# Kernel optimization log

Hardware: AMD Instinct MI355X
Metric: run time of the kernel (lower is better)

## Reference

```python
import jax, jax.numpy as jnp
import numpy as np

P, H_OUT, D, NX = 32, 1, 256, 16
S_A = -0.1

def layernorm(x, g, b, eps=1e-5):
    mu = jnp.mean(x, axis=-1, keepdims=True)
    var = jnp.var(x, axis=-1, keepdims=True)
    return (x - mu) * jax.lax.rsqrt(var + eps) * g + b

def setup_inputs() -> dict:
    key = jax.random.key(0)
    ks = jax.random.split(key, 16)
    B, L = 8, 2048
    y = jax.random.normal(ks[0], (B, L, P), jnp.float32)
    Win = jax.random.normal(ks[1], (P, D), jnp.float32) / np.sqrt(P)
    bin_ = jnp.zeros((D,), jnp.float32)
    ng = jnp.ones((D,), jnp.float32); nb = jnp.zeros((D,), jnp.float32)
    # A = -10*rand + s_A, with A[:,0] = s_A (fix first state of each channel)
    A = -10.0 * jax.random.uniform(ks[2], (D, NX), jnp.float32) + S_A
    A = A.at[:, 0].set(S_A)
    W_B = jax.random.normal(ks[3], (NX, D), jnp.float32)
    W_C = jax.random.normal(ks[4], (NX, D), jnp.float32)
    q_delta = jax.random.normal(ks[5], (D,), jnp.float32)
    p_delta = jax.random.normal(ks[6], (1,), jnp.float32)
    nfg = jnp.ones((D,), jnp.float32); nfb = jnp.zeros((D,), jnp.float32)
    W1 = jax.random.normal(ks[7], (D, D), jnp.float32) / np.sqrt(D)
    b1 = jnp.zeros((D,), jnp.float32)
    W2 = jax.random.normal(ks[8], (D, H_OUT * P), jnp.float32) / np.sqrt(D)
    b2 = jnp.zeros((H_OUT * P,), jnp.float32)
    return {"y": y, "Win": Win, "bin_": bin_, "ng": ng, "nb": nb, "A": A,
            "W_B": W_B, "W_C": W_C, "q_delta": q_delta, "p_delta": p_delta,
            "nfg": nfg, "nfb": nfb, "W1": W1, "b1": b1, "W2": W2, "b2": b2}

def selective_scan(u, delta, A, Bm, Cm):
    # u: (B,L,D), delta: (B,L), A: (D,NX), Bm/Cm: (B,L,NX)
    dA = jnp.exp(delta[..., None, None] * A)                      # (B,L,D,NX)
    dBu = delta[..., None, None] * Bm[:, :, None, :] * u[..., None]  # (B,L,D,NX)
    x0 = jnp.zeros((u.shape[0], u.shape[2], A.shape[1]), u.dtype)
    def step(x, inp):
        dA_t, dBu_t, C_t = inp
        x = dA_t * x + dBu_t                                      # (B,D,NX)
        y_t = jnp.einsum('bdn,bn->bd', x, C_t)
        return x, y_t
    _, ys = jax.lax.scan(step, x0, (dA.transpose(1, 0, 2, 3),
                                    dBu.transpose(1, 0, 2, 3),
                                    Cm.transpose(1, 0, 2)))
    return ys.transpose(1, 0, 2)                                  # (B,L,D)

def reference(y, Win, bin_, ng, nb, A, W_B, W_C, q_delta, p_delta,
              nfg, nfb, W1, b1, W2, b2):
    B, L, _ = y.shape
    h = y @ Win + bin_                                            # (B,L,D)
    hn = layernorm(h, ng, nb)
    delta = jax.nn.softplus(p_delta[0] + jnp.einsum('bld,d->bl', hn, q_delta))
    Bm = jnp.einsum('nd,bld->bln', W_B, hn)
    Cm = jnp.einsum('nd,bld->bln', W_C, hn)
    upd = selective_scan(hn, delta, A, Bm, Cm)
    h = h + upd
    h = layernorm(h, nfg, nfb)
    out = jax.nn.gelu(h @ W1 + b1, approximate=False) @ W2 + b2
    return out.reshape(B, L, H_OUT, P)
```

## Files before the change

### kernel.cpp

```cpp
#include <hip/hip_runtime.h>
#include <math.h>

#define D 256
#define NX 16
#define L 2048
#define NBATCH 8
#define NTOK (NBATCH * L)
#define CL 32
#define NCH (L / CL)
#define LOG2E 1.44269504088896340736f

typedef float f32x4 __attribute__((ext_vector_type(4)));
typedef short bf16x8 __attribute__((ext_vector_type(8)));

__device__ __forceinline__ unsigned short f2bf(float x) {
  unsigned u = __float_as_uint(x);
  u = u + 0x7fffu + ((u >> 16) & 1u);
  return (unsigned short)(u >> 16);
}
__device__ __forceinline__ float bf2f(unsigned short h) {
  return __uint_as_float(((unsigned)h) << 16);
}

__global__ __launch_bounds__(256) void k0_prep(const float* __restrict__ A,
                                               const float* __restrict__ WB,
                                               const float* __restrict__ WC,
                                               const float* __restrict__ W1,
                                               const float* __restrict__ W2,
                                               float* __restrict__ At,
                                               float* __restrict__ Wbct,
                                               unsigned short* __restrict__ W1fh,
                                               unsigned short* __restrict__ W1fl,
                                               unsigned short* __restrict__ W2fh,
                                               unsigned short* __restrict__ W2fl) {
  int i = blockIdx.x * 256 + threadIdx.x;
  if (i < 4096) {
    int d = i >> 4, n = i & 15;
    At[n * D + d] = A[i] * LOG2E;
  } else if (i < 12288) {
    int j = i - 4096;
    int d = j >> 5, c = j & 31;
    Wbct[j] = (c < 16) ? WB[c * D + d] : WC[(c - 16) * D + d];
  } else if (i < 77824) {
    int e = i - 12288;
    int j = e & 7, l = (e >> 3) & 63, tt = (e >> 9) & 15, s = e >> 13;
    int k = s * 32 + ((l >> 4) << 3) + j;
    int n = tt * 16 + (l & 15);
    float x = W1[k * 256 + n];
    unsigned short h = f2bf(x);
    W1fh[e] = h;
    W1fl[e] = f2bf(x - bf2f(h));
  } else {
    int e = i - 77824;
    int j = e & 7, l = (e >> 3) & 63, tt = (e >> 9) & 1, s = e >> 10;
    int k = s * 32 + ((l >> 4) << 3) + j;
    int n = tt * 16 + (l & 15);
    float x = W2[k * 32 + n];
    unsigned short h = f2bf(x);
    W2fh[e] = h;
    W2fl[e] = f2bf(x - bf2f(h));
  }
}

__global__ __launch_bounds__(512, 4) void k1a_front_scan(
    const float* __restrict__ y, const float* __restrict__ Win,
    const float* __restrict__ bin_, const float* __restrict__ ng,
    const float* __restrict__ nb, const float* __restrict__ Wbct,
    const float* __restrict__ qd, const float* __restrict__ pd,
    const float* __restrict__ At,
    float* __restrict__ hn, float* __restrict__ delta,
    float* __restrict__ Bm, float* __restrict__ Cm,
    float* __restrict__ muv, float* __restrict__ irsv,
    float* __restrict__ EX, float* __restrict__ T) {
  __shared__ float sy[32][32];
  __shared__ float sh[32][260];
  __shared__ float sB[32][NX];
  __shared__ float sdelta[32];
  __shared__ float sph[2 * 32 * 32];
  int t = threadIdx.x;
  int tok0 = blockIdx.x * 32;
  if (t < 256) {
    const float4* src = (const float4*)(y + (size_t)tok0 * 32);
    ((float4*)sy)[t] = src[t];
  }
  __syncthreads();
  int dcol = t & 63;
  int jrow = t >> 6;
  int d4 = dcol * 4;
  float4 bv = ((const float4*)bin_)[dcol];
  float4 g4 = ((const float4*)ng)[dcol];
  float4 nb4 = ((const float4*)nb)[dcol];
  float4 q4 = ((const float4*)qd)[dcol];
  float pd0 = pd[0];
  const float4* Win4 = (const float4*)Win;
  for (int g = 0; g < 2; ++g) {
    int j0 = jrow * 4 + g * 2;
    float4 acc0 = bv, acc1 = bv;
    #pragma unroll 4
    for (int k = 0; k < 32; ++k) {
      float4 wv = Win4[k * 64 + dcol];
      float a0 = sy[j0][k];
      float a1 = sy[j0 + 1][k];
      acc0.x = fmaf(a0, wv.x, acc0.x); acc1.x = fmaf(a1, wv.x, acc1.x);
      acc0.y = fmaf(a0, wv.y, acc0.y); acc1.y = fmaf(a1, wv.y, acc1.y);
      acc0.z = fmaf(a0, wv.z, acc0.z); acc1.z = fmaf(a1, wv.z, acc1.z);
      acc0.w = fmaf(a0, wv.w, acc0.w); acc1.w = fmaf(a1, wv.w, acc1.w);
    }
    #pragma unroll
    for (int p = 0; p < 2; ++p) {
      int j = j0 + p;
      int tok = tok0 + j;
      float4 a = (p == 0) ? acc0 : acc1;
      float s1 = a.x + a.y + a.z + a.w;
      float s2 = a.x * a.x + a.y * a.y + a.z * a.z + a.w * a.w;
      #pragma unroll
      for (int off = 1; off < 64; off <<= 1) {
        s1 += __shfl_xor(s1, off);
        s2 += __shfl_xor(s2, off);
      }
      float mu = s1 * (1.f / D);
      float var = s2 * (1.f / D) - mu * mu;
      float rstd = rsqrtf(var + 1e-5f);
      if (dcol == 0) { muv[tok] = mu; irsv[tok] = sqrtf(var + 1e-5f); }
      float4 v4;
      v4.x = (a.x - mu) * rstd * g4.x + nb4.x;
      v4.y = (a.y - mu) * rstd * g4.y + nb4.y;
      v4.z = (a.z - mu) * rstd * g4.z + nb4.z;
      v4.w = (a.w - mu) * rstd * g4.w + nb4.w;
      ((float4*)(hn + (size_t)tok * D))[dcol] = v4;
      *(float4*)&sh[j][d4] = v4;
      float dd = v4.x * q4.x + v4.y * q4.y + v4.z * q4.z + v4.w * q4.w;
      #pragma unroll
      for (int off = 1; off < 64; off <<= 1) dd += __shfl_xor(dd, off);
      if (dcol == 0) {
        float xx = pd0 + dd;
        float dv = (xx > 20.f) ? xx : log1pf(expf(xx));
        delta[tok] = dv;
        sdelta[j] = dv;
      }
    }
  }
  __syncthreads();
  if (t < 32) {
    float v = sdelta[t];
    #pragma unroll
    for (int off = 1; off < 32; off <<= 1) v += __shfl_xor(v, off);
    if (t == 0) T[blockIdx.x] = v;
  }
  {
    int hk = t >> 8;
    int r = t & 255;
    int col4 = r & 7;
    int j = r >> 3;
    const float* shrow = &sh[j][hk * 128];
    const float4* W4 = (const float4*)Wbct + (size_t)hk * 128 * 8;
    float4 o = make_float4(0.f, 0.f, 0.f, 0.f);
    #pragma unroll 4
    for (int k = 0; k < 128; ++k) {
      float av = shrow[k];
      float4 wv = W4[k * 8 + col4];
      o.x = fmaf(av, wv.x, o.x);
      o.y = fmaf(av, wv.y, o.y);
      o.z = fmaf(av, wv.z, o.z);
      o.w = fmaf(av, wv.w, o.w);
    }
    *(float4*)&sph[((hk * 32 + j) << 5) + col4 * 4] = o;
  }
  __syncthreads();
  if (t < 256) {
    int j = t >> 3, cc = t & 7;
    float4 r0 = *(float4*)&sph[(j << 5) + cc * 4];
    float4 r1 = *(float4*)&sph[((32 + j) << 5) + cc * 4];
    float4 r;
    r.x = r0.x + r1.x; r.y = r0.y + r1.y;
    r.z = r0.z + r1.z; r.w = r0.w + r1.w;
    int tokj = tok0 + j;
    if (cc < 4) {
      ((float4*)(Bm + (size_t)tokj * NX))[cc] = r;
      *(float4*)&sB[j][cc * 4] = r;
    } else {
      ((float4*)(Cm + (size_t)tokj * NX))[cc - 4] = r;
    }
  }
  __syncthreads();
  {
    int half = t >> 8;
    int d = t & 255;
    float a8[8], x8[8];
    #pragma unroll
    for (int n = 0; n < 8; ++n) {
      a8[n] = At[(half * 8 + n) * D + d];
      x8[n] = 0.f;
    }
    for (int lo = 0; lo < CL; ++lo) {
      float dlt = sdelta[lo];
      float du = dlt * sh[lo][d];
      #pragma unroll
      for (int n = 0; n < 8; ++n)
        x8[n] = fmaf(exp2f(dlt * a8[n]), x8[n], du * sB[lo][half * 8 + n]);
    }
    size_t exbase = (size_t)blockIdx.x * (NX * D) + d;
    #pragma unroll
    for (int n = 0; n < 8; ++n) EX[exbase + (half * 8 + n) * D] = x8[n];
  }
}

__global__ __launch_bounds__(64) void k2b_chunkscan(
    const float* __restrict__ At, const float* __restrict__ T,
    float* __restrict__ EX) {
  __shared__ float sT[NCH];
  int b = blockIdx.x >> 6;
  int rem = ((blockIdx.x & 63) << 6) | threadIdx.x;
  sT[threadIdx.x] = T[b * NCH + threadIdx.x];
  __syncthreads();
  float A2 = At[rem];
  size_t base = ((size_t)b << 18) + rem;
  float eq[8];
  #pragma unroll
  for (int j = 0; j < 8; ++j) eq[j] = EX[base + ((size_t)j << 12)];
  float x = 0.f;
  #pragma unroll 8
  for (int c = 0; c < NCH; ++c) {
    float e = eq[c & 7];
    if (c + 8 < NCH) eq[c & 7] = EX[base + ((size_t)(c + 8) << 12)];
    EX[base + ((size_t)c << 12)] = x;
    x = fmaf(exp2f(sT[c] * A2), x, e);
  }
}

__device__ __forceinline__ float gelu_exact(float x) {
  return 0.5f * x * (1.f + erff(x * 0.70710678118654752440f));
}

__global__ __launch_bounds__(256) void k2cd_scan_mlp(
    const float* __restrict__ hn, const float* __restrict__ delta,
    const float* __restrict__ Bm, const float* __restrict__ Cm,
    const float* __restrict__ At, const float* __restrict__ EX,
    const float* __restrict__ muv, const float* __restrict__ irsv,
    const float* __restrict__ ng, const float* __restrict__ nb,
    const float* __restrict__ nfg, const float* __restrict__ nfb,
    const unsigned short* __restrict__ W1fh, const unsigned short* __restrict__ W1fl,
    const unsigned short* __restrict__ W2fh, const unsigned short* __restrict__ W2fl,
    const float* __restrict__ b1, const float* __restrict__ b2,
    float* __restrict__ out) {
  __shared__ float s_az[32 * 260];
  __shared__ __align__(16) unsigned short sAh[32 * 256];
  __shared__ __align__(16) unsigned short sAl[32 * 256];
  __shared__ float sB[32][NX];
  __shared__ float sC[32][NX];
  __shared__ float sdelta[32];
  __shared__ float smu[32];
  __shared__ float sirs[32];
  int t = threadIdx.x;
  int tok0 = blockIdx.x * 32;
  size_t tokbase = (size_t)tok0;
  if (t < 32) {
    sdelta[t] = delta[tokbase + t];
    smu[t] = muv[tokbase + t];
    sirs[t] = irsv[tokbase + t];
  }
  for (int i = t; i < 32 * NX; i += 256) {
    ((float*)sB)[i] = Bm[tokbase * NX + i];
    ((float*)sC)[i] = Cm[tokbase * NX + i];
  }
  float a16[16], x16[16];
  size_t exbase = (size_t)blockIdx.x * (NX * D) + t;
  #pragma unroll
  for (int n = 0; n < 16; ++n) {
    a16[n] = At[n * D + t];
    x16[n] = EX[exbase + n * D];
  }
  float nb_d = nb[t];
  float invg = 1.0f / ng[t];
  __syncthreads();
  for (int lo = 0; lo < CL; ++lo) {
    float hv = hn[(tokbase + lo) * D + t];
    float dlt = sdelta[lo];
    float du = dlt * hv;
    float p = 0.f;
    #pragma unroll
    for (int n = 0; n < 16; ++n) {
      x16[n] = fmaf(exp2f(dlt * a16[n]), x16[n], du * sB[lo][n]);
      p = fmaf(x16[n], sC[lo][n], p);
    }
    float h = fmaf((hv - nb_d) * invg, sirs[lo], smu[lo]);
    s_az[lo * 260 + t] = h + p;
  }
  __syncthreads();
  int dcol = t & 63, jrow = t >> 6;
  int d4 = dcol * 4, j8 = jrow * 8;
  {
    float4 g4 = ((const float4*)nfg)[dcol];
    float4 b4 = ((const float4*)nfb)[dcol];
    for (int jj = 0; jj < 8; ++jj) {
      int lo = j8 + jj;
      float4 v = *(float4*)&s_az[lo * 260 + d4];
      float s1 = v.x + v.y + v.z + v.w;
      float s2 = v.x * v.x + v.y * v.y + v.z * v.z + v.w * v.w;
      #pragma unroll
      for (int off = 1; off < 64; off <<= 1) {
        s1 += __shfl_xor(s1, off);
        s2 += __shfl_xor(s2, off);
      }
      float mu2 = s1 * (1.f / D);
      float var2 = s2 * (1.f / D) - mu2 * mu2;
      float rstd2 = rsqrtf(var2 + 1e-5f);
      float4 o;
      o.x = (v.x - mu2) * rstd2 * g4.x + b4.x;
      o.y = (v.y - mu2) * rstd2 * g4.y + b4.y;
      o.z = (v.z - mu2) * rstd2 * g4.z + b4.z;
      o.w = (v.w - mu2) * rstd2 * g4.w + b4.w;
      unsigned short h0 = f2bf(o.x), h1 = f2bf(o.y), h2 = f2bf(o.z), h3 = f2bf(o.w);
      unsigned short q0 = f2bf(o.x - bf2f(h0));
      unsigned short q1 = f2bf(o.y - bf2f(h1));
      unsigned short q2 = f2bf(o.z - bf2f(h2));
      unsigned short q3 = f2bf(o.w - bf2f(h3));
      unsigned off16 = ((unsigned)(d4 * 2)) ^ ((unsigned)(lo & 7) << 4);
      uint2 hv2, lv2;
      hv2.x = (unsigned)h0 | ((unsigned)h1 << 16);
      hv2.y = (unsigned)h2 | ((unsigned)h3 << 16);
      lv2.x = (unsigned)q0 | ((unsigned)q1 << 16);
      lv2.y = (unsigned)q2 | ((unsigned)q3 << 16);
      *(uint2*)((char*)sAh + lo * 512 + off16) = hv2;
      *(uint2*)((char*)sAl + lo * 512 + off16) = lv2;
    }
  }
  __syncthreads();
  int l = t & 63, w = t >> 6;
  const bf16x8* B1h = (const bf16x8*)W1fh;
  const bf16x8* B1l = (const bf16x8*)W1fl;
  f32x4 acc[2][4];
  #pragma unroll
  for (int m = 0; m < 2; ++m)
    #pragma unroll
    for (int n = 0; n < 4; ++n) {
      f32x4 z4 = {0.f, 0.f, 0.f, 0.f};
      acc[m][n] = z4;
    }
  #pragma unroll 2
  for (int s = 0; s < 8; ++s) {
    bf16x8 ah[2], al[2];
    #pragma unroll
    for (int m = 0; m < 2; ++m) {
      int row = m * 16 + (l & 15);
      unsigned off16 = ((unsigned)(s * 64 + ((l >> 4) << 4))) ^ ((unsigned)(row & 7) << 4);
      ah[m] = *(const bf16x8*)((const char*)sAh + row * 512 + off16);
      al[m] = *(const bf16x8*)((const char*)sAl + row * 512 + off16);
    }
    #pragma unroll
    for (int n = 0; n < 4; ++n) {
      int bi = (s * 16 + w * 4 + n) * 64 + l;
      bf16x8 bh = B1h[bi];
      bf16x8 bl = B1l[bi];
      #pragma unroll
      for (int m = 0; m < 2; ++m) {
        acc[m][n] = __builtin_amdgcn_mfma_f32_16x16x32_bf16(ah[m], bh, acc[m][n], 0, 0, 0);
        acc[m][n] = __builtin_amdgcn_mfma_f32_16x16x32_bf16(al[m], bh, acc[m][n], 0, 0, 0);
        acc[m][n] = __builtin_amdgcn_mfma_f32_16x16x32_bf16(ah[m], bl, acc[m][n], 0, 0, 0);
        acc[m][n] = __builtin_amdgcn_mfma_f32_16x16x32_bf16(al[m], bl, acc[m][n], 0, 0, 0);
      }
    }
  }
  __syncthreads();
  #pragma unroll
  for (int n = 0; n < 4; ++n) {
    int colz = w * 64 + n * 16 + (l & 15);
    float b1v = b1[colz];
    #pragma unroll
    for (int m = 0; m < 2; ++m) {
      #pragma unroll
      for (int r = 0; r < 4; ++r) {
        int row = m * 16 + ((l >> 4) << 2) + r;
        float zv = gelu_exact(acc[m][n][r] + b1v);
        unsigned short zh = f2bf(zv);
        unsigned short zl = f2bf(zv - bf2f(zh));
        unsigned off16 = ((unsigned)(colz * 2)) ^ ((unsigned)(row & 7) << 4);
        *(unsigned short*)((char*)sAh + row * 512 + off16) = zh;
        *(unsigned short*)((char*)sAl + row * 512 + off16) = zl;
      }
    }
  }
  __syncthreads();
  int mw = w >> 1, nw = w & 1;
  const bf16x8* B2h = (const bf16x8*)W2fh;
  const bf16x8* B2l = (const bf16x8*)W2fl;
  f32x4 acc2 = {0.f, 0.f, 0.f, 0.f};
  #pragma unroll 2
  for (int s = 0; s < 8; ++s) {
    int row = mw * 16 + (l & 15);
    unsigned off16 = ((unsigned)(s * 64 + ((l >> 4) << 4))) ^ ((unsigned)(row & 7) << 4);
    bf16x8 zh8 = *(const bf16x8*)((const char*)sAh + row * 512 + off16);
    bf16x8 zl8 = *(const bf16x8*)((const char*)sAl + row * 512 + off16);
    int bi = (s * 2 + nw) * 64 + l;
    bf16x8 bh = B2h[bi];
    bf16x8 bl = B2l[bi];
    acc2 = __builtin_amdgcn_mfma_f32_16x16x32_bf16(zh8, bh, acc2, 0, 0, 0);
    acc2 = __builtin_amdgcn_mfma_f32_16x16x32_bf16(zl8, bh, acc2, 0, 0, 0);
    acc2 = __builtin_amdgcn_mfma_f32_16x16x32_bf16(zh8, bl, acc2, 0, 0, 0);
    acc2 = __builtin_amdgcn_mfma_f32_16x16x32_bf16(zl8, bl, acc2, 0, 0, 0);
  }
  int colo = nw * 16 + (l & 15);
  float b2v = b2[colo];
  #pragma unroll
  for (int r = 0; r < 4; ++r) {
    int row = mw * 16 + ((l >> 4) << 2) + r;
    out[(size_t)(tok0 + row) * 32 + colo] = acc2[r] + b2v;
  }
}

extern "C" void kernel_launch(void* const* d_in, const int* in_sizes, int n_in,
                              void* d_out, int out_size, void* d_ws, size_t ws_size,
                              hipStream_t stream) {
  const float* y    = (const float*)d_in[0];
  const float* Win  = (const float*)d_in[1];
  const float* bin_ = (const float*)d_in[2];
  const float* ng   = (const float*)d_in[3];
  const float* nb   = (const float*)d_in[4];
  const float* A    = (const float*)d_in[5];
  const float* WB   = (const float*)d_in[6];
  const float* WC   = (const float*)d_in[7];
  const float* qd   = (const float*)d_in[8];
  const float* pd   = (const float*)d_in[9];
  const float* nfg  = (const float*)d_in[10];
  const float* nfb  = (const float*)d_in[11];
  const float* W1   = (const float*)d_in[12];
  const float* b1   = (const float*)d_in[13];
  const float* W2   = (const float*)d_in[14];
  const float* b2   = (const float*)d_in[15];

  float* ws = (float*)d_ws;
  float* hnbuf = ws;
  float* delta = ws + 4194304;
  float* Bm    = delta + NTOK;
  float* Cm    = Bm + NTOK * NX;
  float* muv   = Cm + NTOK * NX;
  float* irsv  = muv + NTOK;
  float* Tbuf  = irsv + NTOK;
  float* At    = Tbuf + NBATCH * NCH;
  float* Wbct  = At + D * NX;
  float* EX    = Wbct + D * 32;
  unsigned short* W1fh = (unsigned short*)(EX + 2097152);
  unsigned short* W1fl = W1fh + 65536;
  unsigned short* W2fh = W1fl + 65536;
  unsigned short* W2fl = W2fh + 8192;

  k0_prep<<<336, 256, 0, stream>>>(A, WB, WC, W1, W2, At, Wbct,
                                   W1fh, W1fl, W2fh, W2fl);
  k1a_front_scan<<<NTOK / 32, 512, 0, stream>>>(y, Win, bin_, ng, nb, Wbct,
                                                qd, pd, At, hnbuf, delta, Bm,
                                                Cm, muv, irsv, EX, Tbuf);
  k2b_chunkscan<<<NBATCH * 64, 64, 0, stream>>>(At, Tbuf, EX);
  k2cd_scan_mlp<<<NTOK / 32, 256, 0, stream>>>(hnbuf, delta, Bm, Cm, At, EX,
                                               muv, irsv, ng, nb, nfg, nfb,
                                               W1fh, W1fl, W2fh, W2fl,
                                               b1, b2, (float*)d_out);
}
```

Measured before the change: 199.4 us.

## Move front-end input projection and B/C projection onto split-bf16 MFMA

Replaces the scalar FMA input projection (y@Win) and the hn@[W_B;W_C] projection in the front-scan kernel with 16x16x32 bf16 MFMA using hi/lo bf16 splits (four MFMAs per tile) to keep near-fp32 accuracy. The prep kernel now builds pre-swizzled hi/lo bf16 fragments for Win and W_B/W_C. LayerNorm statistics and the delta dot product are reduced through shared memory across waves, and hn is staged into XOR-swizzled bf16 shared buffers for the second GEMM. The aim is to cut ALU time in the front kernel, at the cost of extra conversions, more shared memory (which may lower occupancy) and more barriers.

```diff
diff --git a/kernel.cpp b/kernel.cpp
--- a/kernel.cpp
+++ b/kernel.cpp
@@ -25,24 +25,43 @@
 __global__ __launch_bounds__(256) void k0_prep(const float* __restrict__ A,
                                                const float* __restrict__ WB,
                                                const float* __restrict__ WC,
+                                               const float* __restrict__ Win,
                                                const float* __restrict__ W1,
                                                const float* __restrict__ W2,
                                                float* __restrict__ At,
-                                               float* __restrict__ Wbct,
                                                unsigned short* __restrict__ W1fh,
                                                unsigned short* __restrict__ W1fl,
                                                unsigned short* __restrict__ W2fh,
-                                               unsigned short* __restrict__ W2fl) {
+                                               unsigned short* __restrict__ W2fl,
+                                               unsigned short* __restrict__ Winfh,
+                                               unsigned short* __restrict__ Winfl,
+                                               unsigned short* __restrict__ Wbcfh,
+                                               unsigned short* __restrict__ Wbcfl) {
   int i = blockIdx.x * 256 + threadIdx.x;
   if (i < 4096) {
     int d = i >> 4, n = i & 15;
     At[n * D + d] = A[i] * LOG2E;
   } else if (i < 12288) {
-    int j = i - 4096;
-    int d = j >> 5, c = j & 31;
-    Wbct[j] = (c < 16) ? WB[c * D + d] : WC[(c - 16) * D + d];
-  } else if (i < 77824) {
+    int e = i - 4096;
+    int j = e & 7, l = (e >> 3) & 63, tt = e >> 9;
+    int k = ((l >> 4) << 3) + j;
+    int n = tt * 16 + (l & 15);
+    float x = Win[k * 256 + n];
+    unsigned short h = f2bf(x);
+    Winfh[e] = h;
+    Winfl[e] = f2bf(x - bf2f(h));
+  } else if (i < 20480) {
     int e = i - 12288;
+    int j = e & 7, l = (e >> 3) & 63, q = e >> 9;
+    int s = q >> 1, tt = q & 1;
+    int k = s * 32 + ((l >> 4) << 3) + j;
+    int n = tt * 16 + (l & 15);
+    float x = (n < 16) ? WB[n * 256 + k] : WC[(n - 16) * 256 + k];
+    unsigned short h = f2bf(x);
+    Wbcfh[e] = h;
+    Wbcfl[e] = f2bf(x - bf2f(h));
+  } else if (i < 86016) {
+    int e = i - 20480;
     int j = e & 7, l = (e >> 3) & 63, tt = (e >> 9) & 15, s = e >> 13;
     int k = s * 32 + ((l >> 4) << 3) + j;
     int n = tt * 16 + (l & 15);
@@ -51,7 +70,7 @@
     W1fh[e] = h;
     W1fl[e] = f2bf(x - bf2f(h));
   } else {
-    int e = i - 77824;
+    int e = i - 86016;
     int j = e & 7, l = (e >> 3) & 63, tt = (e >> 9) & 1, s = e >> 10;
     int k = s * 32 + ((l >> 4) << 3) + j;
     int n = tt * 16 + (l & 15);
@@ -63,123 +82,225 @@
 }
 
 __global__ __launch_bounds__(512, 4) void k1a_front_scan(
-    const float* __restrict__ y, const float* __restrict__ Win,
-    const float* __restrict__ bin_, const float* __restrict__ ng,
-    const float* __restrict__ nb, const float* __restrict__ Wbct,
+    const float* __restrict__ y, const float* __restrict__ bin_,
+    const float* __restrict__ ng, const float* __restrict__ nb,
     const float* __restrict__ qd, const float* __restrict__ pd,
     const float* __restrict__ At,
+    const unsigned short* __restrict__ Winfh,
+    const unsigned short* __restrict__ Winfl,
+    const unsigned short* __restrict__ Wbcfh,
+    const unsigned short* __restrict__ Wbcfl,
     float* __restrict__ hn, float* __restrict__ delta,
     float* __restrict__ Bm, float* __restrict__ Cm,
     float* __restrict__ muv, float* __restrict__ irsv,
     float* __restrict__ EX, float* __restrict__ T) {
-  __shared__ float sy[32][32];
+  __shared__ float sy[32][36];
   __shared__ float sh[32][260];
   __shared__ float sB[32][NX];
+  __shared__ float sred[32][16];
   __shared__ float sdelta[32];
-  __shared__ float sph[2 * 32 * 32];
+  __shared__ float smu[32];
+  __shared__ float srstd[32];
+  __shared__ __align__(16) unsigned short sChA_h[32 * 256];
+  __shared__ __align__(16) unsigned short sChA_l[32 * 256];
   int t = threadIdx.x;
+  int l = t & 63;
+  int w = t >> 6;
   int tok0 = blockIdx.x * 32;
   if (t < 256) {
-    const float4* src = (const float4*)(y + (size_t)tok0 * 32);
-    ((float4*)sy)[t] = src[t];
-  }
-  __syncthreads();
-  int dcol = t & 63;
-  int jrow = t >> 6;
-  int d4 = dcol * 4;
-  float4 bv = ((const float4*)bin_)[dcol];
-  float4 g4 = ((const float4*)ng)[dcol];
-  float4 nb4 = ((const float4*)nb)[dcol];
-  float4 q4 = ((const float4*)qd)[dcol];
-  float pd0 = pd[0];
-  const float4* Win4 = (const float4*)Win;
-  for (int g = 0; g < 2; ++g) {
-    int j0 = jrow * 4 + g * 2;
-    float4 acc0 = bv, acc1 = bv;
-    #pragma unroll 4
-    for (int k = 0; k < 32; ++k) {
-      float4 wv = Win4[k * 64 + dcol];
-      float a0 = sy[j0][k];
-      float a1 = sy[j0 + 1][k];
-      acc0.x = fmaf(a0, wv.x, acc0.x); acc1.x = fmaf(a1, wv.x, acc1.x);
-      acc0.y = fmaf(a0, wv.y, acc0.y); acc1.y = fmaf(a1, wv.y, acc1.y);
-      acc0.z = fmaf(a0, wv.z, acc0.z); acc1.z = fmaf(a1, wv.z, acc1.z);
-      acc0.w = fmaf(a0, wv.w, acc0.w); acc1.w = fmaf(a1, wv.w, acc1.w);
-    }
-    #pragma unroll
-    for (int p = 0; p < 2; ++p) {
-      int j = j0 + p;
-      int tok = tok0 + j;
-      float4 a = (p == 0) ? acc0 : acc1;
-      float s1 = a.x + a.y + a.z + a.w;
-      float s2 = a.x * a.x + a.y * a.y + a.z * a.z + a.w * a.w;
-      #pragma unroll
-      for (int off = 1; off < 64; off <<= 1) {
-        s1 += __shfl_xor(s1, off);
-        s2 += __shfl_xor(s2, off);
-      }
-      float mu = s1 * (1.f / D);
-      float var = s2 * (1.f / D) - mu * mu;
-      float rstd = rsqrtf(var + 1e-5f);
-      if (dcol == 0) { muv[tok] = mu; irsv[tok] = sqrtf(var + 1e-5f); }
-      float4 v4;
-      v4.x = (a.x - mu) * rstd * g4.x + nb4.x;
-      v4.y = (a.y - mu) * rstd * g4.y + nb4.y;
-      v4.z = (a.z - mu) * rstd * g4.z + nb4.z;
-      v4.w = (a.w - mu) * rstd * g4.w + nb4.w;
-      ((float4*)(hn + (size_t)tok * D))[dcol] = v4;
-      *(float4*)&sh[j][d4] = v4;
-      float dd = v4.x * q4.x + v4.y * q4.y + v4.z * q4.z + v4.w * q4.w;
-      #pragma unroll
-      for (int off = 1; off < 64; off <<= 1) dd += __shfl_xor(dd, off);
-      if (dcol == 0) {
-        float xx = pd0 + dd;
-        float dv = (xx > 20.f) ? xx : log1pf(expf(xx));
-        delta[tok] = dv;
-        sdelta[j] = dv;
-      }
-    }
+    int row = t >> 3, c4 = t & 7;
+    *(float4*)&sy[row][c4 * 4] = ((const float4*)(y + (size_t)tok0 * 32))[t];
+  }
+  __syncthreads();
+  f32x4 acc[2][2];
+  {
+    bf16x8 yah[2], yal[2];
+    int k0 = (l >> 4) << 3;
+    #pragma unroll
+    for (int m = 0; m < 2; ++m) {
+      int row = m * 16 + (l & 15);
+      float4 f0 = *(float4*)&sy[row][k0];
+      float4 f1 = *(float4*)&sy[row][k0 + 4];
+      float v0 = f0.x, v1 = f0.y, v2 = f0.z, v3 = f0.w;
+      float v4 = f1.x, v5 = f1.y, v6 = f1.z, v7 = f1.w;
+      unsigned short h0 = f2bf(v0), h1 = f2bf(v1), h2 = f2bf(v2), h3 = f2bf(v3);
+      unsigned short h4 = f2bf(v4), h5 = f2bf(v5), h6 = f2bf(v6), h7 = f2bf(v7);
+      yah[m][0] = (short)h0; yah[m][1] = (short)h1; yah[m][2] = (short)h2; yah[m][3] = (short)h3;
+      yah[m][4] = (short)h4; yah[m][5] = (short)h5; yah[m][6] = (short)h6; yah[m][7] = (short)h7;
+      yal[m][0] = (short)f2bf(v0 - bf2f(h0)); yal[m][1] = (short)f2bf(v1 - bf2f(h1));
+      yal[m][2] = (short)f2bf(v2 - bf2f(h2)); yal[m][3] = (short)f2bf(v3 - bf2f(h3));
+      yal[m][4] = (short)f2bf(v4 - bf2f(h4)); yal[m][5] = (short)f2bf(v5 - bf2f(h5));
+      yal[m][6] = (short)f2bf(v6 - bf2f(h6)); yal[m][7] = (short)f2bf(v7 - bf2f(h7));
+    }
+    const bf16x8* Bh = (const bf16x8*)Winfh;
+    const bf16x8* Bl = (const bf16x8*)Winfl;
+    #pragma unroll
+    for (int n = 0; n < 2; ++n) {
+      int tt = w * 2 + n;
+      bf16x8 bh = Bh[tt * 64 + l];
+      bf16x8 bl = Bl[tt * 64 + l];
+      #pragma unroll
+      for (int m = 0; m < 2; ++m) {
+        f32x4 a = {0.f, 0.f, 0.f, 0.f};
+        a = __builtin_amdgcn_mfma_f32_16x16x32_bf16(yah[m], bh, a, 0, 0, 0);
+        a = __builtin_amdgcn_mfma_f32_16x16x32_bf16(yal[m], bh, a, 0, 0, 0);
+        a = __builtin_amdgcn_mfma_f32_16x16x32_bf16(yah[m], bl, a, 0, 0, 0);
+        a = __builtin_amdgcn_mfma_f32_16x16x32_bf16(yal[m], bl, a, 0, 0, 0);
+        acc[m][n] = a;
+      }
+    }
+  }
+  int c0 = w * 32 + (l & 15), c1 = c0 + 16;
+  {
+    float b0 = bin_[c0], b1v = bin_[c1];
+    #pragma unroll
+    for (int m = 0; m < 2; ++m)
+      #pragma unroll
+      for (int r = 0; r < 4; ++r) { acc[m][0][r] += b0; acc[m][1][r] += b1v; }
+  }
+  {
+    #pragma unroll
+    for (int m = 0; m < 2; ++m)
+      #pragma unroll
+      for (int r = 0; r < 4; ++r) {
+        float a0 = acc[m][0][r], a1 = acc[m][1][r];
+        float s1 = a0 + a1;
+        float s2 = a0 * a0 + a1 * a1;
+        #pragma unroll
+        for (int off = 1; off < 16; off <<= 1) {
+          s1 += __shfl_xor(s1, off);
+          s2 += __shfl_xor(s2, off);
+        }
+        if ((l & 15) == 0) {
+          int tok = m * 16 + ((l >> 4) << 2) + r;
+          sred[tok][w * 2] = s1;
+          sred[tok][w * 2 + 1] = s2;
+        }
+      }
   }
   __syncthreads();
   if (t < 32) {
-    float v = sdelta[t];
-    #pragma unroll
-    for (int off = 1; off < 32; off <<= 1) v += __shfl_xor(v, off);
-    if (t == 0) T[blockIdx.x] = v;
-  }
-  {
-    int hk = t >> 8;
-    int r = t & 255;
-    int col4 = r & 7;
-    int j = r >> 3;
-    const float* shrow = &sh[j][hk * 128];
-    const float4* W4 = (const float4*)Wbct + (size_t)hk * 128 * 8;
-    float4 o = make_float4(0.f, 0.f, 0.f, 0.f);
-    #pragma unroll 4
-    for (int k = 0; k < 128; ++k) {
-      float av = shrow[k];
-      float4 wv = W4[k * 8 + col4];
-      o.x = fmaf(av, wv.x, o.x);
-      o.y = fmaf(av, wv.y, o.y);
-      o.z = fmaf(av, wv.z, o.z);
-      o.w = fmaf(av, wv.w, o.w);
-    }
-    *(float4*)&sph[((hk * 32 + j) << 5) + col4 * 4] = o;
-  }
-  __syncthreads();
-  if (t < 256) {
-    int j = t >> 3, cc = t & 7;
-    float4 r0 = *(float4*)&sph[(j << 5) + cc * 4];
-    float4 r1 = *(float4*)&sph[((32 + j) << 5) + cc * 4];
-    float4 r;
-    r.x = r0.x + r1.x; r.y = r0.y + r1.y;
-    r.z = r0.z + r1.z; r.w = r0.w + r1.w;
-    int tokj = tok0 + j;
-    if (cc < 4) {
-      ((float4*)(Bm + (size_t)tokj * NX))[cc] = r;
-      *(float4*)&sB[j][cc * 4] = r;
+    float s1 = 0.f, s2 = 0.f;
+    #pragma unroll
+    for (int q = 0; q < 8; ++q) { s1 += sred[t][q * 2]; s2 += sred[t][q * 2 + 1]; }
+    float mu = s1 * (1.f / D);
+    float var = s2 * (1.f / D) - mu * mu;
+    float rstd = rsqrtf(var + 1e-5f);
+    smu[t] = mu;
+    srstd[t] = rstd;
+    muv[tok0 + t] = mu;
+    irsv[tok0 + t] = sqrtf(var + 1e-5f);
+  }
+  __syncthreads();
+  {
+    float g0 = ng[c0], g1 = ng[c1];
+    float nb0 = nb[c0], nb1 = nb[c1];
+    float q0 = qd[c0], q1 = qd[c1];
+    float ddv[2][4];
+    #pragma unroll
+    for (int m = 0; m < 2; ++m)
+      #pragma unroll
+      for (int r = 0; r < 4; ++r) {
+        int tok = m * 16 + ((l >> 4) << 2) + r;
+        float mu = smu[tok], rstd = srstd[tok];
+        float h0 = (acc[m][0][r] - mu) * rstd * g0 + nb0;
+        float h1 = (acc[m][1][r] - mu) * rstd * g1 + nb1;
+        sh[tok][c0] = h0;
+        sh[tok][c1] = h1;
+        float dx = h0 * q0 + h1 * q1;
+        #pragma unroll
+        for (int off = 1; off < 16; off <<= 1) dx += __shfl_xor(dx, off);
+        ddv[m][r] = dx;
+      }
+    if ((l & 15) == 0) {
+      #pragma unroll
+      for (int m = 0; m < 2; ++m)
+        #pragma unroll
+        for (int r = 0; r < 4; ++r)
+          sred[m * 16 + ((l >> 4) << 2) + r][w] = ddv[m][r];
+    }
+  }
+  __syncthreads();
+  if (t < 32) {
+    float dsum = 0.f;
+    #pragma unroll
+    for (int q = 0; q < 8; ++q) dsum += sred[t][q];
+    float xx = pd[0] + dsum;
+    float dv = (xx > 20.f) ? xx : log1pf(expf(xx));
+    delta[tok0 + t] = dv;
+    sdelta[t] = dv;
+    float tv = dv;
+    #pragma unroll
+    for (int off = 1; off < 32; off <<= 1) tv += __shfl_xor(tv, off);
+    if (t == 0) T[blockIdx.x] = tv;
+  }
+  {
+    int row = t & 31;
+    int cq = (t >> 5) * 16;
+    float4 f0 = *(float4*)&sh[row][cq];
+    float4 f1 = *(float4*)&sh[row][cq + 4];
+    float4 f2 = *(float4*)&sh[row][cq + 8];
+    float4 f3 = *(float4*)&sh[row][cq + 12];
+    float vv[16] = {f0.x, f0.y, f0.z, f0.w, f1.x, f1.y, f1.z, f1.w,
+                    f2.x, f2.y, f2.z, f2.w, f3.x, f3.y, f3.z, f3.w};
+    unsigned hw[8], lw[8];
+    #pragma unroll
+    for (int p = 0; p < 8; ++p) {
+      unsigned short ha = f2bf(vv[2 * p]), hb = f2bf(vv[2 * p + 1]);
+      unsigned short la = f2bf(vv[2 * p] - bf2f(ha));
+      unsigned short lb = f2bf(vv[2 * p + 1] - bf2f(hb));
+      hw[p] = (unsigned)ha | ((unsigned)hb << 16);
+      lw[p] = (unsigned)la | ((unsigned)lb << 16);
+    }
+    unsigned base = (unsigned)row * 512;
+    #pragma unroll
+    for (int g = 0; g < 2; ++g) {
+      unsigned off = ((unsigned)(cq * 2 + g * 16)) ^ ((unsigned)(row & 7) << 4);
+      uint4 hv4 = {hw[g * 4], hw[g * 4 + 1], hw[g * 4 + 2], hw[g * 4 + 3]};
+      uint4 lv4 = {lw[g * 4], lw[g * 4 + 1], lw[g * 4 + 2], lw[g * 4 + 3]};
+      *(uint4*)((char*)sChA_h + base + off) = hv4;
+      *(uint4*)((char*)sChA_l + base + off) = lv4;
+    }
+  }
+  __syncthreads();
+  if (w < 4) {
+    int mw = w & 1, nw = w >> 1;
+    int row = mw * 16 + (l & 15);
+    unsigned abase = (unsigned)row * 512;
+    const bf16x8* B2h = (const bf16x8*)Wbcfh;
+    const bf16x8* B2l = (const bf16x8*)Wbcfl;
+    f32x4 acc2 = {0.f, 0.f, 0.f, 0.f};
+    #pragma unroll
+    for (int s = 0; s < 8; ++s) {
+      unsigned off = ((unsigned)(s * 64 + ((l >> 4) << 4))) ^ ((unsigned)(row & 7) << 4);
+      bf16x8 ah = *(const bf16x8*)((const char*)sChA_h + abase + off);
+      bf16x8 al = *(const bf16x8*)((const char*)sChA_l + abase + off);
+      int bi = (s * 2 + nw) * 64 + l;
+      bf16x8 bh = B2h[bi];
+      bf16x8 bl = B2l[bi];
+      acc2 = __builtin_amdgcn_mfma_f32_16x16x32_bf16(ah, bh, acc2, 0, 0, 0);
+      acc2 = __builtin_amdgcn_mfma_f32_16x16x32_bf16(al, bh, acc2, 0, 0, 0);
+      acc2 = __builtin_amdgcn_mfma_f32_16x16x32_bf16(ah, bl, acc2, 0, 0, 0);
+      acc2 = __builtin_amdgcn_mfma_f32_16x16x32_bf16(al, bl, acc2, 0, 0, 0);
+    }
+    int tokr = mw * 16 + ((l >> 4) << 2);
+    int colc = l & 15;
+    if (nw == 0) {
+      #pragma unroll
+      for (int r = 0; r < 4; ++r) {
+        Bm[(size_t)(tok0 + tokr + r) * NX + colc] = acc2[r];
+        sB[tokr + r][colc] = acc2[r];
+      }
     } else {
-      ((float4*)(Cm + (size_t)tokj * NX))[cc - 4] = r;
+      #pragma unroll
+      for (int r = 0; r < 4; ++r)
+        Cm[(size_t)(tok0 + tokr + r) * NX + colc] = acc2[r];
+    }
+  } else {
+    float4* dst = (float4*)(hn + (size_t)tok0 * D);
+    for (int i = t - 256; i < 2048; i += 256) {
+      int row = i >> 6, c4 = i & 63;
+      dst[i] = *(float4*)&sh[row][c4 * 4];
     }
   }
   __syncthreads();
@@ -437,18 +558,23 @@
   float* irsv  = muv + NTOK;
   float* Tbuf  = irsv + NTOK;
   float* At    = Tbuf + NBATCH * NCH;
-  float* Wbct  = At + D * NX;
-  float* EX    = Wbct + D * 32;
-  unsigned short* W1fh = (unsigned short*)(EX + 2097152);
-  unsigned short* W1fl = W1fh + 65536;
-  unsigned short* W2fh = W1fl + 65536;
-  unsigned short* W2fl = W2fh + 8192;
-
-  k0_prep<<<336, 256, 0, stream>>>(A, WB, WC, W1, W2, At, Wbct,
-                                   W1fh, W1fl, W2fh, W2fl);
-  k1a_front_scan<<<NTOK / 32, 512, 0, stream>>>(y, Win, bin_, ng, nb, Wbct,
-                                                qd, pd, At, hnbuf, delta, Bm,
-                                                Cm, muv, irsv, EX, Tbuf);
+  float* EX    = At + D * NX;
+  unsigned short* W1fh  = (unsigned short*)(EX + 2097152);
+  unsigned short* W1fl  = W1fh + 65536;
+  unsigned short* W2fh  = W1fl + 65536;
+  unsigned short* W2fl  = W2fh + 8192;
+  unsigned short* Winfh = W2fl + 8192;
+  unsigned short* Winfl = Winfh + 8192;
+  unsigned short* Wbcfh = Winfl + 8192;
+  unsigned short* Wbcfl = Wbcfh + 8192;
+
+  k0_prep<<<368, 256, 0, stream>>>(A, WB, WC, Win, W1, W2, At,
+                                   W1fh, W1fl, W2fh, W2fl,
+                                   Winfh, Winfl, Wbcfh, Wbcfl);
+  k1a_front_scan<<<NTOK / 32, 512, 0, stream>>>(y, bin_, ng, nb, qd, pd, At,
+                                                Winfh, Winfl, Wbcfh, Wbcfl,
+                                                hnbuf, delta, Bm, Cm,
+                                                muv, irsv, EX, Tbuf);
   k2b_chunkscan<<<NBATCH * 64, 64, 0, stream>>>(At, Tbuf, EX);
   k2cd_scan_mlp<<<NTOK / 32, 256, 0, stream>>>(hnbuf, delta, Bm, Cm, At, EX,
                                                muv, irsv, ng, nb, nfg, nfb,
```

New measurement: 182.1 us. 8.7% less time.
